# Optimization experiments

Measured on AMD Instinct MI355X. Metric: run time of the kernel, lower is better.

## Reference

```python
import jax, jax.numpy as jnp
import numpy as np

B, S, D = 32, 512, 512
GH, LH = 8, 4            # global / local num_heads
W, STRIDE = 10, 5        # local window size and hop (window_size // 2)


def _mha(x, w_in, b_in, w_out, b_out, n_heads, key_mask=None):
    """Torch nn.MultiheadAttention (self-attn, eval mode). x: [N, L, D]."""
    N, L, d = x.shape
    dh = d // n_heads
    qkv = x @ w_in.T + b_in                       # [N, L, 3D]
    q, k, v = jnp.split(qkv, 3, axis=-1)
    def heads(t):
        return t.reshape(N, L, n_heads, dh).transpose(0, 2, 1, 3)  # [N,H,L,dh]
    q, k, v = heads(q), heads(k), heads(v)
    scores = jnp.einsum('bhqd,bhkd->bhqk', q, k) / jnp.sqrt(jnp.asarray(dh, x.dtype))
    if key_mask is not None:                      # key_mask: [N, L] bool, True = valid
        scores = jnp.where(key_mask[:, None, None, :], scores, jnp.asarray(-1e9, x.dtype))
    attn = jax.nn.softmax(scores, axis=-1)
    out = jnp.einsum('bhqk,bhkd->bhqd', attn, v).transpose(0, 2, 1, 3).reshape(N, L, d)
    return out @ w_out.T + b_out


def setup_inputs() -> dict:
    key = jax.random.key(0)
    ks = jax.random.split(key, 12)
    s = 0.02
    return {
        'x':      jax.random.normal(ks[0], (B, S, D), jnp.float32),
        'gw_in':  jax.random.normal(ks[1], (3 * D, D), jnp.float32) * s,
        'gb_in':  jnp.zeros((3 * D,), jnp.float32),
        'gw_out': jax.random.normal(ks[2], (D, D), jnp.float32) * s,
        'gb_out': jnp.zeros((D,), jnp.float32),
        'lw_in':  jax.random.normal(ks[3], (3 * D, D), jnp.float32) * s,
        'lb_in':  jnp.zeros((3 * D,), jnp.float32),
        'lw_out': jax.random.normal(ks[4], (D, D), jnp.float32) * s,
        'lb_out': jnp.zeros((D,), jnp.float32),
        'fw':     jax.random.normal(ks[5], (D, 2 * D), jnp.float32) * s,
        'fb':     jnp.zeros((D,), jnp.float32),
    }


def reference(x, gw_in, gb_in, gw_out, gb_out, lw_in, lb_in, lw_out, lb_out, fw, fb):
    # ---- global branch: full self-attention over the sequence ----
    global_out = _mha(x, gw_in, gb_in, gw_out, gb_out, GH)

    # ---- local branch: overlapping windows of size W, hop STRIDE ----
    starts = np.arange(0, S, STRIDE)              # static window starts
    NW = len(starts)
    pos = starts[:, None] + np.arange(W)          # [NW, W] absolute positions
    valid = pos < S                               # ragged tail windows
    idx = np.minimum(pos, S - 1)                  # clipped gather indices

    windows = x[:, idx]                           # [B, NW, W, D]
    windows = windows.reshape(B * NW, W, D)
    key_mask = jnp.broadcast_to(jnp.asarray(valid)[None], (B, NW, W)).reshape(B * NW, W)

    local_attn = _mha(windows, lw_in, lb_in, lw_out, lb_out, LH, key_mask=key_mask)
    local_attn = local_attn.reshape(B, NW, W, D) * jnp.asarray(valid)[None, :, :, None].astype(x.dtype)

    # scatter-add overlapping window outputs back (matches `local_out[:, i:end] +=`)
    local_out = jnp.zeros_like(x).at[:, idx.reshape(-1)].add(local_attn.reshape(B, NW * W, D))

    # ---- fusion MLP (dropout = identity in eval) ----
    combined = jnp.concatenate([global_out, local_out], axis=-1)   # [B, S, 2D]
    return jax.nn.relu(combined @ fw.T + fb)
```

## Files before the change

### kernel.cpp

```cpp
#include <hip/hip_runtime.h>
#include <cstdint>
#include <cstddef>

#define DEV __device__ __forceinline__

typedef float f32x4 __attribute__((ext_vector_type(4)));
typedef short bf16x8 __attribute__((ext_vector_type(8)));

DEV unsigned short f2bf(float f) {
  union { float f; unsigned u; } v; v.f = f;
  unsigned u = v.u;
  unsigned r = u + 0x7FFFu + ((u >> 16) & 1u);
  return (unsigned short)(r >> 16);
}
DEV unsigned short f2bf_hu(float f) {
  union { float f; unsigned u; } v; v.f = f;
  return (unsigned short)((v.u + 0x8000u) >> 16);
}
DEV float bf2f(unsigned short h) {
  union { unsigned u; float f; } v; v.u = ((unsigned)h) << 16;
  return v.f;
}

DEV void gload16(const void* g, void* l) {
  __builtin_amdgcn_global_load_lds((const __attribute__((address_space(1))) unsigned int*)g,
                                   (__attribute__((address_space(3))) unsigned int*)l,
                                   16, 0, 0);
}

DEV f32x4 MFMA(bf16x8 a, bf16x8 b, f32x4 c) {
  return __builtin_amdgcn_mfma_f32_16x16x32_bf16(a, b, c, 0, 0, 0);
}

__global__ void k_f2bf(const float* __restrict__ src, unsigned short* __restrict__ dst, int n) {
  int i = (blockIdx.x * blockDim.x + threadIdx.x) * 4;
  int stride = gridDim.x * blockDim.x * 4;
  for (; i < n; i += stride) {
    float4 v = *(const float4*)(src + i);
    ushort4 o;
    o.x = f2bf(v.x); o.y = f2bf(v.y); o.z = f2bf(v.z); o.w = f2bf(v.w);
    *(ushort4*)(dst + i) = o;
  }
}

__global__ __launch_bounds__(256) void k_merge(const float* __restrict__ fw,
                                               const float* __restrict__ gw_out,
                                               const float* __restrict__ lw_out,
                                               unsigned short* __restrict__ M1b,
                                               unsigned short* __restrict__ M2b) {
  __shared__ float Fa[64][68];
  __shared__ float Gb[64][68];
  const int bi = blockIdx.x, bj = blockIdx.y, m2 = blockIdx.z;
  const float* g = m2 ? lw_out : gw_out;
  const int i0 = bi * 64, j0 = bj * 64;
  const int tid = threadIdx.x;
  const int tr = tid >> 4, tc = tid & 15;
  float acc[4][4] = {};
  for (int kc = 0; kc < 8; kc++) {
    int k0 = kc * 64;
    __syncthreads();
    #pragma unroll
    for (int it = 0; it < 4; it++) {
      int r = tr + 16 * it;
      float4 v = *(const float4*)(fw + (size_t)(i0 + r) * 1024 + m2 * 512 + k0 + tc * 4);
      Fa[tc * 4 + 0][r] = v.x; Fa[tc * 4 + 1][r] = v.y;
      Fa[tc * 4 + 2][r] = v.z; Fa[tc * 4 + 3][r] = v.w;
      *(float4*)&Gb[r][tc * 4] = *(const float4*)(g + (size_t)(k0 + r) * 512 + j0 + tc * 4);
    }
    __syncthreads();
    for (int k = 0; k < 64; k++) {
      float4 a4 = *(const float4*)&Fa[k][tr * 4];
      float4 b4 = *(const float4*)&Gb[k][tc * 4];
      float av[4] = {a4.x, a4.y, a4.z, a4.w};
      float bv[4] = {b4.x, b4.y, b4.z, b4.w};
      #pragma unroll
      for (int r = 0; r < 4; r++)
        #pragma unroll
        for (int c = 0; c < 4; c++)
          acc[r][c] += av[r] * bv[c];
    }
  }
  unsigned short* M = m2 ? M2b : M1b;
  #pragma unroll
  for (int r = 0; r < 4; r++) {
    ushort4 pk;
    pk.x = f2bf(acc[r][0]); pk.y = f2bf(acc[r][1]);
    pk.z = f2bf(acc[r][2]); pk.w = f2bf(acc[r][3]);
    *(ushort4*)&M[(size_t)(i0 + tr * 4 + r) * 512 + j0 + tc * 4] = pk;
  }
}

__global__ __launch_bounds__(256) void k_bias(const float* __restrict__ fw, const float* __restrict__ gb_out,
                                              const float* __restrict__ lb_out, const float* __restrict__ fb,
                                              float* __restrict__ bias1, float* __restrict__ bias2) {
  __shared__ float bv[512];
  const int which = blockIdx.y;
  const int i0 = blockIdx.x * 64;
  const float* src = which ? lb_out : gb_out;
  for (int t = threadIdx.x; t < 512; t += 256) bv[t] = src[t];
  __syncthreads();
  const int r = threadIdx.x >> 2, c4 = threadIdx.x & 3;
  const float* frow = fw + (size_t)(i0 + r) * 1024 + (which ? 512 : 0) + c4 * 128;
  float a = 0.f;
  #pragma unroll 4
  for (int k = 0; k < 128; k += 4) {
    float4 v = *(const float4*)(frow + k);
    a += v.x * bv[c4 * 128 + k] + v.y * bv[c4 * 128 + k + 1]
       + v.z * bv[c4 * 128 + k + 2] + v.w * bv[c4 * 128 + k + 3];
  }
  a += __shfl_xor(a, 1);
  a += __shfl_xor(a, 2);
  if (c4 == 0) {
    int i = i0 + r;
    if (which) bias2[i] = a;
    else       bias1[i] = a + fb[i];
  }
}

template <int EPI>
__global__ __launch_bounds__(256) void k_gemm(const unsigned short* __restrict__ A,
                                              const unsigned short* __restrict__ A2,
                                              const unsigned short* __restrict__ Wm,
                                              const unsigned short* __restrict__ W2,
                                              const float* __restrict__ bias,
                                              const float* __restrict__ bias2,
                                              float qscale, void* __restrict__ Cout,
                                              int Ntot, int NT) {
  __shared__ unsigned short As[2][128 * 32];
  __shared__ unsigned short Bs[2][128 * 32];
  const int tid = threadIdx.x;
  const int wave = tid >> 6, lane = tid & 63;
  const int wr = wave >> 1, wc = wave & 1;
  const int bm = blockIdx.x, bn = blockIdx.y;
  const int ql = lane & 15, kg = lane >> 4;

  const int c0 = wave * 2;
  const int srow = lane >> 2;
  const int sks = (lane & 3) * 8;

  auto stage = [&](int buf, int t) {
    const unsigned short* sA = A;
    const unsigned short* sW = Wm;
    int k0 = t * 32;
    if (EPI == 1 && t >= 16) { sA = A2; sW = W2; k0 = (t - 16) * 32; }
    #pragma unroll
    for (int i = 0; i < 2; i++) {
      int c = c0 + i;
      int row = c * 16 + srow;
      gload16(sA + (size_t)(bm * 128 + row) * 512 + k0 + sks, &As[buf][c * 512 + lane * 8]);
      gload16(sW + (size_t)(bn * 128 + row) * 512 + k0 + sks, &Bs[buf][c * 512 + lane * 8]);
    }
  };

  f32x4 acc[4][4] = {};
  stage(0, 0);
  __syncthreads();
  for (int t = 0; t < NT; t++) {
    int buf = t & 1;
    if (t + 1 < NT) stage(buf ^ 1, t + 1);
    const unsigned short* as = As[buf];
    const unsigned short* bs = Bs[buf];
    bf16x8 af[4], bfr[4];
    #pragma unroll
    for (int m = 0; m < 4; m++)
      af[m] = *(const bf16x8*)&as[(wr * 64 + m * 16 + ql) * 32 + kg * 8];
    #pragma unroll
    for (int n = 0; n < 4; n++)
      bfr[n] = *(const bf16x8*)&bs[(wc * 64 + n * 16 + ql) * 32 + kg * 8];
    #pragma unroll
    for (int m = 0; m < 4; m++)
      #pragma unroll
      for (int n = 0; n < 4; n++)
        acc[m][n] = MFMA(af[m], bfr[n], acc[m][n]);
    __syncthreads();
  }

  const int row0 = bm * 128 + wr * 64;
  const int col0 = bn * 128 + wc * 64;
  if (EPI == 0) {
    unsigned short* C = (unsigned short*)Cout;
    #pragma unroll
    for (int m = 0; m < 4; m++)
      #pragma unroll
      for (int n = 0; n < 4; n++) {
        int col = col0 + n * 16 + ql;
        float bcol = bias[col];
        float qs = (col < 512) ? qscale : 1.0f;
        #pragma unroll
        for (int r = 0; r < 4; r++) {
          int row = row0 + m * 16 + kg * 4 + r;
          C[(size_t)row * Ntot + col] = f2bf((acc[m][n][r] + bcol) * qs);
        }
      }
  } else {
    float* C = (float*)Cout;
    #pragma unroll
    for (int m = 0; m < 4; m++)
      #pragma unroll
      for (int n = 0; n < 4; n++) {
        int col = col0 + n * 16 + ql;
        float b1 = bias[col], b2 = bias2[col];
        #pragma unroll
        for (int r = 0; r < 4; r++) {
          int row = row0 + m * 16 + kg * 4 + r;
          float cc = ((row & 511) < 5) ? 1.0f : 2.0f;
          float v = acc[m][n][r] + b1 + cc * b2;
          C[(size_t)row * 512 + col] = fmaxf(v, 0.0f);
        }
      }
  }
}

__global__ __launch_bounds__(512, 2) void k_attn_g(const unsigned short* __restrict__ QKV,
                                                   unsigned short* __restrict__ Og) {
  __shared__ unsigned short Klds[512 * 64];
  __shared__ unsigned short Vt[64][536];
  __shared__ unsigned short Plds[8][16 * 72];
  const int tid = threadIdx.x, wave = tid >> 6, lane = tid & 63;
  const int ql = lane & 15, kg = lane >> 4;
  const int h = blockIdx.x, b = blockIdx.y;
  const size_t tb = (size_t)b * 512;
  const size_t hoff = (size_t)h * 64;

  #pragma unroll
  for (int i = 0; i < 8; i++) {
    int instr = wave * 8 + i;
    int row = instr * 8 + (lane >> 3);
    int slot = lane & 7;
    int c = slot ^ (row & 7);
    gload16(QKV + (tb + row) * 1536 + 512 + hoff + c * 8, &Klds[instr * 512 + lane * 8]);
  }
  {
    const unsigned short* Vp = QKV + (tb + tid) * 1536 + 1024 + hoff;
    #pragma unroll
    for (int c8 = 0; c8 < 8; c8++) {
      bf16x8 v8 = *(const bf16x8*)(Vp + c8 * 8);
      #pragma unroll
      for (int j = 0; j < 8; j++) Vt[c8 * 8 + j][tid] = (unsigned short)v8[j];
    }
  }
  bf16x8 qf[4][2];
  #pragma unroll
  for (int m = 0; m < 4; m++) {
    const unsigned short* Qp = QKV + (tb + wave * 64 + m * 16 + ql) * 1536 + hoff;
    qf[m][0] = *(const bf16x8*)(Qp + kg * 8);
    qf[m][1] = *(const bf16x8*)(Qp + 32 + kg * 8);
  }
  __syncthreads();

  float l_part[4][4] = {};
  f32x4 o[4][4] = {};
  unsigned short* P = &Plds[wave][0];

  for (int kv = 0; kv < 8; kv++) {
    const int k0 = kv * 64;
    bf16x8 kf[4][2], vb[4][2];
    #pragma unroll
    for (int f = 0; f < 4; f++) {
      int row = k0 + 16 * f + ql;
      #pragma unroll
      for (int c = 0; c < 2; c++)
        kf[f][c] = *(const bf16x8*)&Klds[row * 64 + (((c * 4 + kg) ^ (row & 7)) * 8)];
      #pragma unroll
      for (int st = 0; st < 2; st++)
        vb[f][st] = *(const bf16x8*)&Vt[16 * f + ql][k0 + st * 32 + kg * 8];
    }
    #pragma unroll
    for (int m = 0; m < 4; m++) {
      f32x4 s[4] = {};
      #pragma unroll
      for (int f = 0; f < 4; f++) {
        s[f] = MFMA(qf[m][0], kf[f][0], s[f]);
        s[f] = MFMA(qf[m][1], kf[f][1], s[f]);
      }
      #pragma unroll
      for (int f = 0; f < 4; f++)
        #pragma unroll
        for (int r = 0; r < 4; r++)
          s[f][r] = exp2f(s[f][r]);
      #pragma unroll
      for (int r = 0; r < 4; r++)
        l_part[m][r] += (s[0][r] + s[1][r]) + (s[2][r] + s[3][r]);
      #pragma unroll
      for (int f = 0; f < 4; f++) {
        int chunk = (2 * f + (ql >> 3)) ^ kg;
        #pragma unroll
        for (int r = 0; r < 4; r++)
          P[(kg * 4 + r) * 72 + chunk * 8 + (ql & 7)] = f2bf_hu(s[f][r]);
      }
      #pragma unroll
      for (int st = 0; st < 2; st++) {
        bf16x8 pa = *(const bf16x8*)&P[ql * 72 + (((st * 4 + kg) ^ (ql >> 2)) * 8)];
        #pragma unroll
        for (int f = 0; f < 4; f++)
          o[m][f] = MFMA(pa, vb[f][st], o[m][f]);
      }
    }
  }

  #pragma unroll
  for (int m = 0; m < 4; m++)
    #pragma unroll
    for (int r = 0; r < 4; r++) {
      float l = l_part[m][r];
      l += __shfl_xor(l, 1);
      l += __shfl_xor(l, 2);
      l += __shfl_xor(l, 4);
      l += __shfl_xor(l, 8);
      float inv = 1.0f / l;
      size_t row = tb + wave * 64 + m * 16 + kg * 4 + r;
      #pragma unroll
      for (int f = 0; f < 4; f++)
        Og[row * 512 + hoff + 16 * f + ql] = f2bf(o[m][f][r] * inv);
    }
}

__global__ __launch_bounds__(256) void k_attn_l(const unsigned short* __restrict__ QKV,
                                                unsigned short* __restrict__ Lacc) {
  __shared__ unsigned short Qs[5][520];
  __shared__ unsigned short Ks[15][520];
  __shared__ unsigned short Vs[15][520];
  __shared__ float Pb[4][2][5][12];
  __shared__ float Lbuf[5][512];
  const int w = blockIdx.x, b = blockIdx.y;
  const int p0 = 5 * w;
  const int tid = threadIdx.x, wave = tid >> 6, lane = tid & 63;
  const size_t tbase = (size_t)b * 512;

  for (int c = tid; c < 35 * 64; c += 256) {
    int row = c >> 6, ch = (c & 63) * 8;
    if (row < 5) {
      int tok = min(p0 + row, 511);
      *(bf16x8*)&Qs[row][ch] = *(const bf16x8*)(QKV + (tbase + tok) * 1536 + ch);
    } else if (row < 20) {
      int rr = row - 5;
      int tok = min(max(p0 - 5 + rr, 0), 511);
      *(bf16x8*)&Ks[rr][ch] = *(const bf16x8*)(QKV + (tbase + tok) * 1536 + 512 + ch);
    } else {
      int rr = row - 20;
      int tok = min(max(p0 - 5 + rr, 0), 511);
      *(bf16x8*)&Vs[rr][ch] = *(const bf16x8*)(QKV + (tbase + tok) * 1536 + 1024 + ch);
    }
  }
  __syncthreads();

  const int win = wave >> 1;
  const bool active = (win == 0) || (w > 0);
  const int q = lane / 10, j = lane - (lane / 10) * 10;

  for (int it = 0; it < 2; it++) {
    int h = (wave & 1) * 2 + it;
    float scv = -1e30f;
    if (active && lane < 50) {
      int qtok = p0 + q;
      int krow = j + (win == 0 ? 5 : 0);
      int ktok = p0 - 5 + krow;
      if (qtok < 512 && ktok >= 0 && ktok < 512) {
        float acc = 0.f;
        const unsigned short* qp = &Qs[q][h * 128];
        const unsigned short* kp = &Ks[krow][h * 128];
        for (int ck = 0; ck < 16; ck++) {
          bf16x8 q8 = *(const bf16x8*)(qp + ck * 8);
          bf16x8 k8 = *(const bf16x8*)(kp + ck * 8);
          #pragma unroll
          for (int e = 0; e < 8; e++)
            acc += bf2f((unsigned short)q8[e]) * bf2f((unsigned short)k8[e]);
        }
        scv = acc;
      }
    }
    if (lane < 50) Pb[wave][it][q][j] = scv;
    if (lane < 50) {
      float mx = -1e30f;
      for (int jj = 0; jj < 10; jj++) mx = fmaxf(mx, Pb[wave][it][q][jj]);
      float su = 0.f;
      for (int jj = 0; jj < 10; jj++) su += exp2f(Pb[wave][it][q][jj] - mx);
      float p = exp2f(scv - mx) / su;
      Pb[wave][it][q][j] = p;
    }
  }
  __syncthreads();

  if (wave < 2) {
    for (int it = 0; it < 2; it++) {
      int h = (wave & 1) * 2 + it;
      for (int qq = 0; qq < 5; qq++) {
        float a0 = 0.f, a1 = 0.f;
        for (int jj = 0; jj < 10; jj++) {
          float p = Pb[wave][it][qq][jj];
          a0 += p * bf2f(Vs[jj + 5][h * 128 + lane]);
          a1 += p * bf2f(Vs[jj + 5][h * 128 + lane + 64]);
        }
        Lbuf[qq][h * 128 + lane] = a0;
        Lbuf[qq][h * 128 + lane + 64] = a1;
      }
    }
  }
  __syncthreads();
  if (wave >= 2 && w > 0) {
    for (int it = 0; it < 2; it++) {
      int h = (wave & 1) * 2 + it;
      for (int qq = 0; qq < 5; qq++) {
        float a0 = 0.f, a1 = 0.f;
        for (int jj = 0; jj < 10; jj++) {
          float p = Pb[wave][it][qq][jj];
          a0 += p * bf2f(Vs[jj][h * 128 + lane]);
          a1 += p * bf2f(Vs[jj][h * 128 + lane + 64]);
        }
        Lbuf[qq][h * 128 + lane] += a0;
        Lbuf[qq][h * 128 + lane + 64] += a1;
      }
    }
  }
  __syncthreads();
  for (int c = tid; c < 5 * 512; c += 256) {
    int qq = c >> 9, d = c & 511;
    int p = p0 + qq;
    if (p < 512) Lacc[(tbase + p) * 512 + d] = f2bf(Lbuf[qq][d]);
  }
}

extern "C" void kernel_launch(void* const* d_in, const int* in_sizes, int n_in,
                              void* d_out, int out_size, void* d_ws, size_t ws_size,
                              hipStream_t stream) {
  const float* x      = (const float*)d_in[0];
  const float* gw_in  = (const float*)d_in[1];
  const float* gb_in  = (const float*)d_in[2];
  const float* gw_out = (const float*)d_in[3];
  const float* gb_out = (const float*)d_in[4];
  const float* lw_in  = (const float*)d_in[5];
  const float* lb_in  = (const float*)d_in[6];
  const float* lw_out = (const float*)d_in[7];
  const float* lb_out = (const float*)d_in[8];
  const float* fw     = (const float*)d_in[9];
  const float* fb     = (const float*)d_in[10];

  char* ws = (char*)d_ws;
  auto alloc = [&](size_t bytes) -> char* {
    char* p = ws;
    ws += (bytes + 255) & ~(size_t)255;
    return p;
  };
  unsigned short* xb     = (unsigned short*)alloc((size_t)16384 * 512 * 2);
  unsigned short* gwin_b = (unsigned short*)alloc((size_t)1536 * 512 * 2);
  unsigned short* lwin_b = (unsigned short*)alloc((size_t)1536 * 512 * 2);
  unsigned short* M1b    = (unsigned short*)alloc((size_t)512 * 512 * 2);
  unsigned short* M2b    = (unsigned short*)alloc((size_t)512 * 512 * 2);
  float* bias1           = (float*)alloc(512 * 4);
  float* bias2           = (float*)alloc(512 * 4);
  unsigned short* QKV    = (unsigned short*)alloc((size_t)16384 * 1536 * 2);
  unsigned short* Og     = (unsigned short*)alloc((size_t)16384 * 512 * 2);
  unsigned short* La     = (unsigned short*)alloc((size_t)16384 * 512 * 2);

  k_f2bf<<<2048, 256, 0, stream>>>(x, xb, 16384 * 512);
  k_f2bf<<<128, 256, 0, stream>>>(gw_in, gwin_b, 1536 * 512);
  k_f2bf<<<128, 256, 0, stream>>>(lw_in, lwin_b, 1536 * 512);
  k_merge<<<dim3(8, 8, 2), 256, 0, stream>>>(fw, gw_out, lw_out, M1b, M2b);
  k_bias<<<dim3(8, 2), 256, 0, stream>>>(fw, gb_out, lb_out, fb, bias1, bias2);

  k_gemm<0><<<dim3(128, 12), 256, 0, stream>>>(xb, nullptr, gwin_b, nullptr, gb_in, nullptr,
                                               0.125f * 1.44269504f, QKV, 1536, 16);
  k_attn_g<<<dim3(8, 32), 512, 0, stream>>>(QKV, Og);

  k_gemm<0><<<dim3(128, 12), 256, 0, stream>>>(xb, nullptr, lwin_b, nullptr, lb_in, nullptr,
                                               0.08838834764831845f * 1.44269504f, QKV, 1536, 16);
  k_attn_l<<<dim3(103, 32), 256, 0, stream>>>(QKV, La);

  k_gemm<1><<<dim3(128, 4), 256, 0, stream>>>(Og, La, M1b, M2b, bias1, bias2,
                                              1.0f, d_out, 512, 32);
}
```

Baseline: 241.6 us.

## Restructure local window attention kernel thread mapping and drop LDS output buffer

Remaps the local-attention kernel so all 400 score dot products are spread across the whole block, followed by a separate 40-thread softmax pass and a PV stage in which each thread owns two output dims and accumulates both windows in registers before a direct packed store. This removes the Lbuf shared buffer, the serialized two-phase accumulation with its extra barriers, and the per-thread redundant softmax recomputation. Masked entries are now zeroed explicitly in the softmax. The risk is a different shared-memory access pattern for the V reads, plus idle threads during the softmax phase.

```diff
diff --git a/kernel.cpp b/kernel.cpp
--- a/kernel.cpp
+++ b/kernel.cpp
@@ -320,11 +320,10 @@
   __shared__ unsigned short Qs[5][520];
   __shared__ unsigned short Ks[15][520];
   __shared__ unsigned short Vs[15][520];
-  __shared__ float Pb[4][2][5][12];
-  __shared__ float Lbuf[5][512];
+  __shared__ float Pb[2][4][5][13];
   const int w = blockIdx.x, b = blockIdx.y;
   const int p0 = 5 * w;
-  const int tid = threadIdx.x, wave = tid >> 6, lane = tid & 63;
+  const int tid = threadIdx.x;
   const size_t tbase = (size_t)b * 512;
 
   for (int c = tid; c < 35 * 64; c += 256) {
@@ -344,21 +343,25 @@
   }
   __syncthreads();
 
-  const int win = wave >> 1;
-  const bool active = (win == 0) || (w > 0);
-  const int q = lane / 10, j = lane - (lane / 10) * 10;
-
-  for (int it = 0; it < 2; it++) {
-    int h = (wave & 1) * 2 + it;
-    float scv = -1e30f;
-    if (active && lane < 50) {
-      int qtok = p0 + q;
-      int krow = j + (win == 0 ? 5 : 0);
+  #pragma unroll
+  for (int rep = 0; rep < 2; rep++) {
+    int idx = tid + rep * 256;
+    if (idx < 400) {
+      int j = idx % 10;
+      int t1 = idx / 10;
+      int q = t1 % 5;
+      int t2 = t1 / 5;
+      int h = t2 & 3;
+      int win = t2 >> 2;
+      int krow = win ? j : j + 5;
       int ktok = p0 - 5 + krow;
-      if (qtok < 512 && ktok >= 0 && ktok < 512) {
+      float scv = -1e30f;
+      bool ok = (win == 0 || w > 0) && (p0 + q < 512) && (ktok < 512);
+      if (ok) {
         float acc = 0.f;
         const unsigned short* qp = &Qs[q][h * 128];
         const unsigned short* kp = &Ks[krow][h * 128];
+        #pragma unroll
         for (int ck = 0; ck < 16; ck++) {
           bf16x8 q8 = *(const bf16x8*)(qp + ck * 8);
           bf16x8 k8 = *(const bf16x8*)(kp + ck * 8);
@@ -368,55 +371,59 @@
         }
         scv = acc;
       }
-    }
-    if (lane < 50) Pb[wave][it][q][j] = scv;
-    if (lane < 50) {
-      float mx = -1e30f;
-      for (int jj = 0; jj < 10; jj++) mx = fmaxf(mx, Pb[wave][it][q][jj]);
-      float su = 0.f;
-      for (int jj = 0; jj < 10; jj++) su += exp2f(Pb[wave][it][q][jj] - mx);
-      float p = exp2f(scv - mx) / su;
-      Pb[wave][it][q][j] = p;
-    }
-  }
-  __syncthreads();
-
-  if (wave < 2) {
-    for (int it = 0; it < 2; it++) {
-      int h = (wave & 1) * 2 + it;
-      for (int qq = 0; qq < 5; qq++) {
-        float a0 = 0.f, a1 = 0.f;
-        for (int jj = 0; jj < 10; jj++) {
-          float p = Pb[wave][it][qq][jj];
-          a0 += p * bf2f(Vs[jj + 5][h * 128 + lane]);
-          a1 += p * bf2f(Vs[jj + 5][h * 128 + lane + 64]);
+      Pb[win][h][q][j] = scv;
+    }
+  }
+  __syncthreads();
+
+  if (tid < 40) {
+    int q = tid % 5;
+    int t2 = tid / 5;
+    int h = t2 & 3;
+    int win = t2 >> 2;
+    float* row = &Pb[win][h][q][0];
+    float mx = -1e30f;
+    #pragma unroll
+    for (int j = 0; j < 10; j++) mx = fmaxf(mx, row[j]);
+    float e[10]; float su = 0.f;
+    #pragma unroll
+    for (int j = 0; j < 10; j++) {
+      float v = row[j];
+      float ej = (v <= -1e29f) ? 0.f : exp2f(v - mx);
+      e[j] = ej; su += ej;
+    }
+    float inv = (su > 0.f) ? 1.0f / su : 0.f;
+    #pragma unroll
+    for (int j = 0; j < 10; j++) row[j] = e[j] * inv;
+  }
+  __syncthreads();
+
+  {
+    const int h = tid >> 6;
+    const int d = tid * 2;
+    for (int qq = 0; qq < 5; qq++) {
+      int p = p0 + qq;
+      if (p >= 512) break;
+      float a0 = 0.f, a1 = 0.f;
+      const float* P0 = &Pb[0][h][qq][0];
+      #pragma unroll
+      for (int j = 0; j < 10; j++) {
+        float pw = P0[j];
+        a0 += pw * bf2f(Vs[j + 5][d]);
+        a1 += pw * bf2f(Vs[j + 5][d + 1]);
+      }
+      if (w > 0) {
+        const float* P1 = &Pb[1][h][qq][0];
+        #pragma unroll
+        for (int j = 0; j < 10; j++) {
+          float pw = P1[j];
+          a0 += pw * bf2f(Vs[j][d]);
+          a1 += pw * bf2f(Vs[j][d + 1]);
         }
-        Lbuf[qq][h * 128 + lane] = a0;
-        Lbuf[qq][h * 128 + lane + 64] = a1;
-      }
-    }
-  }
-  __syncthreads();
-  if (wave >= 2 && w > 0) {
-    for (int it = 0; it < 2; it++) {
-      int h = (wave & 1) * 2 + it;
-      for (int qq = 0; qq < 5; qq++) {
-        float a0 = 0.f, a1 = 0.f;
-        for (int jj = 0; jj < 10; jj++) {
-          float p = Pb[wave][it][qq][jj];
-          a0 += p * bf2f(Vs[jj][h * 128 + lane]);
-          a1 += p * bf2f(Vs[jj][h * 128 + lane + 64]);
-        }
-        Lbuf[qq][h * 128 + lane] += a0;
-        Lbuf[qq][h * 128 + lane + 64] += a1;
-      }
-    }
-  }
-  __syncthreads();
-  for (int c = tid; c < 5 * 512; c += 256) {
-    int qq = c >> 9, d = c & 511;
-    int p = p0 + qq;
-    if (p < 512) Lacc[(tbase + p) * 512 + d] = f2bf(Lbuf[qq][d]);
+      }
+      ushort2 st; st.x = f2bf(a0); st.y = f2bf(a1);
+      *(ushort2*)&Lacc[(tbase + p) * 512 + d] = st;
+    }
   }
 }
 
```

After: 220.4 us. 8.8% less time.
